# Kernel optimization log

Measured on AMD Instinct MI355X. Metric: run time of the kernel, lower is better.

The kernel has to match this reference:

```python
import jax, jax.numpy as jnp
import numpy as np

DIM = 192
HEADS = 4
HID = 576  # dim * ffn_expansion_factor
B, H, W = 8, 128, 128
EPS = 1e-5


def _conv(x, w, b, groups=1, pad=0):
    # x: NCHW, w: OIHW (I = in_channels // groups)
    out = jax.lax.conv_general_dilated(
        x, w, window_strides=(1, 1), padding=[(pad, pad), (pad, pad)],
        dimension_numbers=('NCHW', 'OIHW', 'NCHW'), feature_group_count=groups)
    return out + b[None, :, None, None]


def _layernorm(x, w, b):
    # WithBias LayerNorm over channel dim (equivalent to to_3d -> LN(last) -> to_4d)
    mu = jnp.mean(x, axis=1, keepdims=True)
    var = jnp.mean(jnp.square(x - mu), axis=1, keepdims=True)
    return (x - mu) / jnp.sqrt(var + EPS) * w[None, :, None, None] + b[None, :, None, None]


def _attention(x, qkv_w, qkv_b, qkv_dw_w, qkv_dw_b, temperature, prompt, proj_w, proj_b):
    b, c, h, w = x.shape
    qkv = _conv(_conv(x, qkv_w, qkv_b), qkv_dw_w, qkv_dw_b, groups=3 * DIM, pad=1)
    q, k, v = jnp.split(qkv, 3, axis=1)
    ch = c // HEADS
    hw = h * w
    q = q.reshape(b, HEADS, ch, hw) + prompt  # is_prompt=True: prompt added
    k = k.reshape(b, HEADS, ch, hw) + prompt
    v = v.reshape(b, HEADS, ch, hw) + prompt
    # L2 normalize along spatial (last) axis
    q = q / jnp.maximum(jnp.linalg.norm(q, axis=-1, keepdims=True), 1e-12)
    k = k / jnp.maximum(jnp.linalg.norm(k, axis=-1, keepdims=True), 1e-12)
    attn = jnp.einsum('bhcn,bhdn->bhcd', q, k) * temperature  # [b,heads,ch,ch]
    attn = jax.nn.softmax(attn, axis=-1)
    out = jnp.einsum('bhcd,bhdn->bhcn', attn, v)
    out = out.reshape(b, c, h, w)
    return _conv(out, proj_w, proj_b)


def _ffn(x, dw1_w, dw1_b, pm_w, pm_b, dw2_w, dw2_b, po_w, po_b):
    x1 = _conv(x, dw1_w, dw1_b, groups=DIM, pad=1)       # grouped 3x3: 192 -> 576
    x1 = _conv(x1, pm_w, pm_b)                            # 1x1: 576 -> 576
    x1 = jax.nn.gelu(x1, approximate=False)
    x2 = _conv(x1, dw2_w, dw2_b, groups=HID, pad=1)      # depthwise 3x3
    return _conv(x2, po_w, po_b)                          # 1x1: 576 -> 192


def setup_inputs() -> dict:
    key = jax.random.key(0)
    ks = jax.random.split(key, 24)
    rn = lambda i, shp, s=0.05: jax.random.normal(ks[i], shp, dtype=jnp.float32) * s
    return {
        'x': jax.random.normal(ks[0], (B, DIM, H, W), dtype=jnp.float32),
        'ln1_w': jnp.ones((DIM,), jnp.float32), 'ln1_b': jnp.zeros((DIM,), jnp.float32),
        'qkv_w': rn(1, (3 * DIM, DIM, 1, 1)), 'qkv_b': rn(2, (3 * DIM,)),
        'qkv_dw_w': rn(3, (3 * DIM, 1, 3, 3)), 'qkv_dw_b': rn(4, (3 * DIM,)),
        'temperature': jnp.ones((HEADS, 1, 1), jnp.float32),
        'prompt': jnp.ones((HEADS, DIM // HEADS, 1), jnp.float32),
        'proj_w': rn(5, (DIM, DIM, 1, 1)), 'proj_b': rn(6, (DIM,)),
        'ln2_w': jnp.ones((DIM,), jnp.float32), 'ln2_b': jnp.zeros((DIM,), jnp.float32),
        'ffn_dw1_w': rn(7, (HID, 1, 3, 3)), 'ffn_dw1_b': rn(8, (HID,)),
        'ffn_pm_w': rn(9, (HID, HID, 1, 1)), 'ffn_pm_b': rn(10, (HID,)),
        'ffn_dw2_w': rn(11, (HID, 1, 3, 3)), 'ffn_dw2_b': rn(12, (HID,)),
        'ffn_po_w': rn(13, (DIM, HID, 1, 1)), 'ffn_po_b': rn(14, (DIM,)),
    }


def reference(x, ln1_w, ln1_b, qkv_w, qkv_b, qkv_dw_w, qkv_dw_b, temperature, prompt,
              proj_w, proj_b, ln2_w, ln2_b, ffn_dw1_w, ffn_dw1_b, ffn_pm_w, ffn_pm_b,
              ffn_dw2_w, ffn_dw2_b, ffn_po_w, ffn_po_b):
    x = x + _attention(_layernorm(x, ln1_w, ln1_b), qkv_w, qkv_b, qkv_dw_w, qkv_dw_b,
                       temperature, prompt, proj_w, proj_b)
    x = x + _ffn(_layernorm(x, ln2_w, ln2_b), ffn_dw1_w, ffn_dw1_b, ffn_pm_w, ffn_pm_b,
                 ffn_dw2_w, ffn_dw2_b, ffn_po_w, ffn_po_b)
    return x
```

## Files before the change

### kernel.cpp

```cpp
#include <hip/hip_runtime.h>

#define HW     16384
#define NB     8
#define CDIM   192
#define CH3    576
#define NHEADS 4
#define CHH    48
#define NSL2   128
#define LDP    136
#define KT     64
#define LDK    72


typedef short  v8s  __attribute__((ext_vector_type(8)));
typedef float  v4f  __attribute__((ext_vector_type(4)));
typedef unsigned short u16x8 __attribute__((ext_vector_type(8)));

__device__ __forceinline__ float bf2f(unsigned short s) {
    return __uint_as_float(((unsigned)s) << 16);
}
__device__ __forceinline__ unsigned short f2bf(float f) {
    unsigned u = __float_as_uint(f);
    return (unsigned short)((u + 0x7fffu + ((u >> 16) & 1u)) >> 16);
}
__device__ __forceinline__ float gelu_f(float x) {
    return 0.5f * x * (1.0f + erff(x * 0.70710678118654752f));
}

__global__ __launch_bounds__(256) void wcvt(const float* __restrict__ s0,
                                            const float* __restrict__ s1,
                                            const float* __restrict__ s2,
                                            const float* __restrict__ s3,
                                            const float* __restrict__ dq,
                                            const float* __restrict__ d1,
                                            const float* __restrict__ d2,
                                            unsigned short* __restrict__ d,
                                            int n0, int n1, int n2, int n3) {
    int y = blockIdx.y;
    if (y < 4) {
        const float* srcs[4] = {s0, s1, s2, s3};
        int cnts[4] = {n0, n1, n2, n3};
        int offs[4] = {0, n0, n0 + n1, n0 + n1 + n2};
        const float* s = srcs[y];
        unsigned short* o = d + offs[y];
        int i = (blockIdx.x * 256 + threadIdx.x) * 8;
        if (i + 8 <= cnts[y]) {
            float4 a = *(const float4*)(s + i);
            float4 b = *(const float4*)(s + i + 4);
            u16x8 u;
            u[0] = f2bf(a.x); u[1] = f2bf(a.y); u[2] = f2bf(a.z); u[3] = f2bf(a.w);
            u[4] = f2bf(b.x); u[5] = f2bf(b.y); u[6] = f2bf(b.z); u[7] = f2bf(b.w);
            *(u16x8*)(o + i) = u;
        }
    } else {
        const float* s = (y == 4) ? dq : (y == 5) ? d1 : d2;
        unsigned short* o = d + (n0 + n1 + n2 + n3) + (y - 4) * 9 * CH3;
        int i = blockIdx.x * 256 + threadIdx.x;
        if (i < 9 * CH3) {
            int tap = i / CH3, c = i - tap * CH3;
            o[i] = f2bf(s[c * 9 + tap]);
        }
    }
}

__global__ __launch_bounds__(256) void zero_f(float* __restrict__ p, int n) {
    int i = blockIdx.x * 256 + threadIdx.x;
    if (i < n) p[i] = 0.f;
}

__global__ __launch_bounds__(256) void ln_norm(const float* __restrict__ x,
                                               const float* __restrict__ lnw,
                                               const float* __restrict__ lnb,
                                               unsigned short* __restrict__ xn) {
    int p = blockIdx.x * 256 + threadIdx.x;
    int z = blockIdx.y;
    const float* xp = x + (size_t)z * CDIM * HW;
    float s = 0.f, ss = 0.f;
    for (int c = 0; c < CDIM; ++c) {
        float v = xp[(size_t)c * HW + p];
        s += v; ss += v * v;
    }
    float m = s * (1.0f / CDIM);
    float var = ss * (1.0f / CDIM) - m * m;
    float r = 1.0f / sqrtf(var + 1e-5f);
    unsigned short* op = xn + (size_t)z * HW * CDIM;
    for (int cg = 0; cg < CDIM / 8; ++cg) {
        u16x8 u;
#pragma unroll
        for (int j = 0; j < 8; ++j) {
            int c = cg * 8 + j;
            u[j] = f2bf((xp[(size_t)c * HW + p] - m) * r * lnw[c] + lnb[c]);
        }
        *(u16x8*)(op + (size_t)cg * HW * 8 + (size_t)p * 8) = u;
    }
}

template <int EPI, int K>
__global__ __launch_bounds__(256) void gemm_c8(
    const unsigned short* __restrict__ Wb,
    const unsigned short* __restrict__ X,
    const float* __restrict__ bias,
    unsigned short* __restrict__ out) {
    __shared__ unsigned short Xs[128 * LDK];
    const int t = threadIdx.x;
    const int p0 = blockIdx.x * 128, M0 = blockIdx.y * 192, z = blockIdx.z;
    const int wid = t >> 6, lane = t & 63, lm = lane & 15, quad = lane >> 4;
    const int wp = (wid & 1) * 64, wc = (wid >> 1) * 96;

    const unsigned short* Xz = X + (size_t)z * HW * K;
    const int srow = t >> 1, shalf = (t & 1) * 32;
    const unsigned short* spz = Xz + (size_t)(p0 + srow) * 8;
    unsigned short* sd = &Xs[srow * LDK + shalf];

    v4f acc[4][6];
#pragma unroll
    for (int i = 0; i < 4; ++i)
#pragma unroll
        for (int j = 0; j < 6; ++j) acc[i][j] = (v4f)0.0f;

    const unsigned short* br[6];
#pragma unroll
    for (int j = 0; j < 6; ++j)
        br[j] = Wb + (size_t)(M0 + wc + j * 16 + lm) * K + quad * 8;

    for (int kt = 0; kt < K; kt += KT) {
        int cb = (kt + shalf) >> 3;
        u16x8 g0 = *(const u16x8*)(spz + (size_t)(cb + 0) * HW * 8);
        u16x8 g1 = *(const u16x8*)(spz + (size_t)(cb + 1) * HW * 8);
        u16x8 g2 = *(const u16x8*)(spz + (size_t)(cb + 2) * HW * 8);
        u16x8 g3 = *(const u16x8*)(spz + (size_t)(cb + 3) * HW * 8);
        if (kt) __syncthreads();
        *(u16x8*)sd = g0;
        *(u16x8*)(sd + 8) = g1;
        *(u16x8*)(sd + 16) = g2;
        *(u16x8*)(sd + 24) = g3;
        __syncthreads();
#pragma unroll
        for (int ks = 0; ks < 2; ++ks) {
            v8s a[4], b[6];
#pragma unroll
            for (int i = 0; i < 4; ++i)
                a[i] = *(const v8s*)&Xs[(wp + i * 16 + lm) * LDK + ks * 32 + quad * 8];
#pragma unroll
            for (int j = 0; j < 6; ++j)
                b[j] = *(const v8s*)(br[j] + kt + ks * 32);
#pragma unroll
            for (int i = 0; i < 4; ++i)
#pragma unroll
                for (int j = 0; j < 6; ++j)
                    acc[i][j] = __builtin_amdgcn_mfma_f32_16x16x32_bf16(a[i], b[j], acc[i][j], 0, 0, 0);
        }
    }

    unsigned short* Oz = out + (size_t)z * HW * (size_t)(EPI == 0 ? CH3 : CH3);
#pragma unroll
    for (int i = 0; i < 4; ++i)
#pragma unroll
        for (int j = 0; j < 6; ++j) {
            int ch = M0 + wc + j * 16 + lm;
            int cg = ch >> 3, co = ch & 7;
            float bch = bias[ch];
#pragma unroll
            for (int r = 0; r < 4; ++r) {
                int p = p0 + wp + i * 16 + quad * 4 + r;
                float v = acc[i][j][r] + bch;
                if (EPI == 1) v = gelu_f(v);
                Oz[(size_t)cg * HW * 8 + (size_t)p * 8 + co] = f2bf(v);
            }
        }
}

template <int K>
__global__ __launch_bounds__(256) void gemm_nchw(
    const unsigned short* __restrict__ Wb,
    const unsigned short* __restrict__ X,
    const float* __restrict__ bias,
    const float* __restrict__ res,
    float* __restrict__ outp) {
    __shared__ unsigned short Xs[128 * LDK];
    const int t = threadIdx.x;
    const int p0 = blockIdx.x * 128, z = blockIdx.z;
    const int wid = t >> 6, lane = t & 63, lm = lane & 15, quad = lane >> 4;
    const int wm = (wid >> 1) * 96, wph = (wid & 1) * 64;

    const unsigned short* Xz = X + (size_t)z * HW * K;
    const int srow = t >> 1, shalf = (t & 1) * 32;
    const unsigned short* spz = Xz + (size_t)(p0 + srow) * 8;
    unsigned short* sd = &Xs[srow * LDK + shalf];

    v4f acc[6][4];
#pragma unroll
    for (int i = 0; i < 6; ++i)
#pragma unroll
        for (int j = 0; j < 4; ++j) acc[i][j] = (v4f)0.0f;

    const unsigned short* ar[6];
#pragma unroll
    for (int i = 0; i < 6; ++i)
        ar[i] = Wb + (size_t)(wm + i * 16 + lm) * K + quad * 8;

    for (int kt = 0; kt < K; kt += KT) {
        int cb = (kt + shalf) >> 3;
        u16x8 g0 = *(const u16x8*)(spz + (size_t)(cb + 0) * HW * 8);
        u16x8 g1 = *(const u16x8*)(spz + (size_t)(cb + 1) * HW * 8);
        u16x8 g2 = *(const u16x8*)(spz + (size_t)(cb + 2) * HW * 8);
        u16x8 g3 = *(const u16x8*)(spz + (size_t)(cb + 3) * HW * 8);
        if (kt) __syncthreads();
        *(u16x8*)sd = g0;
        *(u16x8*)(sd + 8) = g1;
        *(u16x8*)(sd + 16) = g2;
        *(u16x8*)(sd + 24) = g3;
        __syncthreads();
#pragma unroll
        for (int ks = 0; ks < 2; ++ks) {
            v8s a[6], b[4];
#pragma unroll
            for (int i = 0; i < 6; ++i)
                a[i] = *(const v8s*)(ar[i] + kt + ks * 32);
#pragma unroll
            for (int j = 0; j < 4; ++j)
                b[j] = *(const v8s*)&Xs[(wph + j * 16 + lm) * LDK + ks * 32 + quad * 8];
#pragma unroll
            for (int i = 0; i < 6; ++i)
#pragma unroll
                for (int j = 0; j < 4; ++j)
                    acc[i][j] = __builtin_amdgcn_mfma_f32_16x16x32_bf16(a[i], b[j], acc[i][j], 0, 0, 0);
        }
    }

#pragma unroll
    for (int i = 0; i < 6; ++i)
#pragma unroll
        for (int j = 0; j < 4; ++j) {
            int gp = p0 + wph + j * 16 + lm;
#pragma unroll
            for (int r = 0; r < 4; ++r) {
                int gm = wm + i * 16 + quad * 4 + r;
                size_t oi = (size_t)z * CDIM * HW + (size_t)gm * HW + gp;
                outp[oi] = acc[i][j][r] + bias[gm] + res[oi];
            }
        }
}

__global__ __launch_bounds__(256) void dwp_c8(const unsigned short* __restrict__ in,
                                              const unsigned short* __restrict__ wT,
                                              const float* __restrict__ b1,
                                              const float* __restrict__ prompt,
                                              unsigned short* __restrict__ out,
                                              float* __restrict__ ssbuf) {
    int t = threadIdx.x;
    int px = blockIdx.x * 256 + t;
    int cg = blockIdx.y, c0 = cg * 8;
    int z = blockIdx.z;
    int h = px >> 7, w = px & 127;
    const unsigned short* ip = in + (size_t)z * HW * CH3 + (size_t)cg * HW * 8;
    int pc = c0 % CDIM;
    float acc[8];
#pragma unroll
    for (int j = 0; j < 8; ++j) acc[j] = b1[c0 + j] + prompt[pc + j];
#pragma unroll
    for (int ky = 0; ky < 3; ++ky) {
        int hy = h + ky - 1;
        if ((unsigned)hy >= 128u) continue;
#pragma unroll
        for (int kx = 0; kx < 3; ++kx) {
            int wx = w + kx - 1;
            if ((unsigned)wx >= 128u) continue;
            u16x8 xv = *(const u16x8*)(ip + (size_t)((hy << 7) + wx) * 8);
            u16x8 wv = *(const u16x8*)(wT + (ky * 3 + kx) * CH3 + c0);
#pragma unroll
            for (int j = 0; j < 8; ++j) acc[j] = fmaf(bf2f(wv[j]), bf2f(xv[j]), acc[j]);
        }
    }
    u16x8 o;
    float sl[8];
#pragma unroll
    for (int j = 0; j < 8; ++j) {
        unsigned short q = f2bf(acc[j]);
        o[j] = q;
        float vr = bf2f(q);
        sl[j] = vr * vr;
    }
    *(u16x8*)(out + (size_t)z * HW * CH3 + (size_t)cg * HW * 8 + (size_t)px * 8) = o;

    if (c0 < 384) {
        int wid = t >> 6, lane = t & 63;
#pragma unroll
        for (int j = 0; j < 8; ++j)
            for (int off = 32; off; off >>= 1) sl[j] += __shfl_down(sl[j], off);
        __shared__ float wr[4][8];
        if (lane == 0)
#pragma unroll
            for (int j = 0; j < 8; ++j) wr[wid][j] = sl[j];
        __syncthreads();
        if (t < 8) {
            float s = wr[0][t] + wr[1][t] + wr[2][t] + wr[3][t];
            atomicAdd(&ssbuf[z * 384 + c0 + t], s);
        }
    }
}

__global__ __launch_bounds__(256) void gram1(const unsigned short* __restrict__ qkvT,
                                             float* __restrict__ G0p) {
    const int sl = blockIdx.x, hh = blockIdx.y, z = blockIdx.z;
    const int t = threadIdx.x;
    const int wid = t >> 6, lane = t & 63, lm = lane & 15, quad = lane >> 4;

    __shared__ float Gs[4][2304];
    unsigned short* qs = (unsigned short*)&Gs[0][0];
    unsigned short* ks = qs + 48 * LDP;

    const unsigned short* bz = qkvT + (size_t)z * HW * CH3;
    int half = t & 1, pl = t >> 1;
    size_t pofs = (size_t)(sl * 128 + pl) * 8;
#pragma unroll
    for (int ci = 0; ci < 3; ++ci) {
        int cg = half * 3 + ci;
        u16x8 uq = *(const u16x8*)(bz + (size_t)(hh * 6 + cg) * HW * 8 + pofs);
        u16x8 uk = *(const u16x8*)(bz + (size_t)(24 + hh * 6 + cg) * HW * 8 + pofs);
#pragma unroll
        for (int j = 0; j < 8; ++j) {
            qs[(cg * 8 + j) * LDP + pl] = uq[j];
            ks[(cg * 8 + j) * LDP + pl] = uk[j];
        }
    }
    __syncthreads();

    v4f acc[3][3];
#pragma unroll
    for (int mi = 0; mi < 3; ++mi)
#pragma unroll
        for (int ni = 0; ni < 3; ++ni) acc[mi][ni] = (v4f)0.0f;

    int kp = wid * 32;
    v8s a[3], b[3];
#pragma unroll
    for (int i = 0; i < 3; ++i) {
        a[i] = *(const v8s*)&qs[(i * 16 + lm) * LDP + kp + quad * 8];
        b[i] = *(const v8s*)&ks[(i * 16 + lm) * LDP + kp + quad * 8];
    }
#pragma unroll
    for (int mi = 0; mi < 3; ++mi)
#pragma unroll
        for (int ni = 0; ni < 3; ++ni)
            acc[mi][ni] = __builtin_amdgcn_mfma_f32_16x16x32_bf16(a[mi], b[ni], acc[mi][ni], 0, 0, 0);

    __syncthreads();
#pragma unroll
    for (int mi = 0; mi < 3; ++mi)
#pragma unroll
        for (int ni = 0; ni < 3; ++ni)
#pragma unroll
            for (int r = 0; r < 4; ++r)
                Gs[wid][(mi * 16 + quad * 4 + r) * 48 + ni * 16 + lm] = acc[mi][ni][r];
    __syncthreads();
    float* gp = G0p + (((size_t)z * NHEADS + hh) * NSL2 + sl) * 2304;
    for (int i = t; i < 2304; i += 256)
        gp[i] = Gs[0][i] + Gs[1][i] + Gs[2][i] + Gs[3][i];
}

__global__ __launch_bounds__(256) void softmax1(const float* __restrict__ G0p,
                                                const float* __restrict__ ssbuf,
                                                const float* __restrict__ temp,
                                                unsigned short* __restrict__ Apad) {
    int hh = blockIdx.x, z = blockIdx.y, t = threadIdx.x;
    __shared__ float Gsum[2304];
    const float* gb = G0p + ((size_t)z * NHEADS + hh) * NSL2 * 2304;
    for (int i = t; i < 2304; i += 256) {
        float s = 0.f;
#pragma unroll 8
        for (int sl = 0; sl < NSL2; ++sl) s += gb[(size_t)sl * 2304 + i];
        Gsum[i] = s;
    }
    __syncthreads();
    if (t < 48) {
        float T = temp[hh];
        const float* sb = ssbuf + z * 384;
        float invq = 1.0f / fmaxf(sqrtf(sb[hh * CHH + t]), 1e-12f);
        float lg[48];
        float mx = -1e30f;
#pragma unroll
        for (int d = 0; d < 48; ++d) {
            float invk = 1.0f / fmaxf(sqrtf(sb[192 + hh * CHH + d]), 1e-12f);
            float l = T * Gsum[t * 48 + d] * invq * invk;
            lg[d] = l;
            mx = fmaxf(mx, l);
        }
        float sum = 0.f;
#pragma unroll
        for (int d = 0; d < 48; ++d) { float e = expf(lg[d] - mx); lg[d] = e; sum += e; }
        float inv = 1.0f / sum;
        unsigned short* ap = Apad + ((size_t)z * NHEADS + hh) * 48 * 64 + t * 64;
#pragma unroll
        for (int d = 0; d < 48; ++d) ap[d] = f2bf(lg[d] * inv);
#pragma unroll
        for (int d = 48; d < 64; ++d) ap[d] = 0;
    }
}

__global__ __launch_bounds__(256) void apply_pv(const unsigned short* __restrict__ qkvT,
                                                const unsigned short* __restrict__ Apad,
                                                unsigned short* __restrict__ attnout) {
    const int t = threadIdx.x;
    const int hh = blockIdx.y, z = blockIdx.z;
    const int wid = t >> 6, lane = t & 63, lm = lane & 15, quad = lane >> 4;
    const int p0 = blockIdx.x * 256 + wid * 64;

    const unsigned short* bz = qkvT + (size_t)z * HW * CH3;
    const unsigned short* Ab = Apad + ((size_t)z * NHEADS + hh) * 48 * 64;

    v4f acc[4][3];
#pragma unroll
    for (int i = 0; i < 4; ++i)
#pragma unroll
        for (int j = 0; j < 3; ++j) acc[i][j] = (v4f)0.0f;

#pragma unroll
    for (int ks = 0; ks < 2; ++ks) {
        int cgv = 48 + hh * 6 + ks * 4 + quad;
        if (cgv > 71) cgv = 71;
        const unsigned short* vp = bz + (size_t)cgv * HW * 8;
        v8s a[4], b[3];
#pragma unroll
        for (int i = 0; i < 4; ++i)
            a[i] = *(const v8s*)(vp + (size_t)(p0 + i * 16 + lm) * 8);
#pragma unroll
        for (int j = 0; j < 3; ++j)
            b[j] = *(const v8s*)(Ab + (j * 16 + lm) * 64 + ks * 32 + quad * 8);
#pragma unroll
        for (int i = 0; i < 4; ++i)
#pragma unroll
            for (int j = 0; j < 3; ++j)
                acc[i][j] = __builtin_amdgcn_mfma_f32_16x16x32_bf16(a[i], b[j], acc[i][j], 0, 0, 0);
    }

    unsigned short* Oz = attnout + (size_t)z * HW * CDIM;
#pragma unroll
    for (int i = 0; i < 4; ++i)
#pragma unroll
        for (int j = 0; j < 3; ++j) {
            int ch = hh * CHH + j * 16 + lm;
            int cg = ch >> 3, co = ch & 7;
#pragma unroll
            for (int r = 0; r < 4; ++r) {
                int p = p0 + i * 16 + quad * 4 + r;
                Oz[(size_t)cg * HW * 8 + (size_t)p * 8 + co] = f2bf(acc[i][j][r]);
            }
        }
}

__global__ __launch_bounds__(256) void dw1_c8(const unsigned short* __restrict__ xn,
                                              const unsigned short* __restrict__ wT,
                                              const float* __restrict__ b1,
                                              unsigned short* __restrict__ f1) {
    int t = threadIdx.x;
    int px = blockIdx.x * 256 + t;
    int gin = blockIdx.y;
    int c0 = gin * 24;
    int z = blockIdx.z;
    int h = px >> 7, w = px & 127;
    const unsigned short* ip = xn + (size_t)z * HW * CDIM + (size_t)gin * HW * 8;
    float acc[24];
#pragma unroll
    for (int j = 0; j < 24; ++j) acc[j] = b1[c0 + j];
#pragma unroll
    for (int ky = 0; ky < 3; ++ky) {
        int hy = h + ky - 1;
        if ((unsigned)hy >= 128u) continue;
#pragma unroll
        for (int kx = 0; kx < 3; ++kx) {
            int wx = w + kx - 1;
            if ((unsigned)wx >= 128u) continue;
            u16x8 xv = *(const u16x8*)(ip + (size_t)((hy << 7) + wx) * 8);
            float mv[8];
#pragma unroll
            for (int j = 0; j < 8; ++j) mv[j] = bf2f(xv[j]);
            const unsigned short* wp = wT + (ky * 3 + kx) * CH3 + c0;
            u16x8 w0 = *(const u16x8*)wp;
            u16x8 w1 = *(const u16x8*)(wp + 8);
            u16x8 w2 = *(const u16x8*)(wp + 16);
            float wv[24];
#pragma unroll
            for (int j = 0; j < 8; ++j) {
                wv[j] = bf2f(w0[j]); wv[8 + j] = bf2f(w1[j]); wv[16 + j] = bf2f(w2[j]);
            }
#pragma unroll
            for (int j = 0; j < 24; ++j) acc[j] = fmaf(wv[j], mv[j / 3], acc[j]);
        }
    }
    unsigned short* f1z = f1 + (size_t)z * HW * CH3;
#pragma unroll
    for (int q8 = 0; q8 < 3; ++q8) {
        u16x8 o;
#pragma unroll
        for (int j = 0; j < 8; ++j) o[j] = f2bf(acc[q8 * 8 + j]);
        *(u16x8*)(f1z + (size_t)(gin * 3 + q8) * HW * 8 + (size_t)px * 8) = o;
    }
}

__global__ __launch_bounds__(256) void dw2_c8(const unsigned short* __restrict__ in,
                                              const unsigned short* __restrict__ wT,
                                              const float* __restrict__ b1,
                                              unsigned short* __restrict__ out) {
    int t = threadIdx.x;
    int px = blockIdx.x * 256 + t;
    int cg = blockIdx.y, c0 = cg * 8;
    int z = blockIdx.z;
    int h = px >> 7, w = px & 127;
    const unsigned short* ip = in + (size_t)z * HW * CH3 + (size_t)cg * HW * 8;
    float acc[8];
#pragma unroll
    for (int j = 0; j < 8; ++j) acc[j] = b1[c0 + j];
#pragma unroll
    for (int ky = 0; ky < 3; ++ky) {
        int hy = h + ky - 1;
        if ((unsigned)hy >= 128u) continue;
#pragma unroll
        for (int kx = 0; kx < 3; ++kx) {
            int wx = w + kx - 1;
            if ((unsigned)wx >= 128u) continue;
            u16x8 xv = *(const u16x8*)(ip + (size_t)((hy << 7) + wx) * 8);
            u16x8 wv = *(const u16x8*)(wT + (ky * 3 + kx) * CH3 + c0);
#pragma unroll
            for (int j = 0; j < 8; ++j) acc[j] = fmaf(bf2f(wv[j]), bf2f(xv[j]), acc[j]);
        }
    }
    u16x8 o;
#pragma unroll
    for (int j = 0; j < 8; ++j) o[j] = f2bf(acc[j]);
    *(u16x8*)(out + (size_t)z * HW * CH3 + (size_t)cg * HW * 8 + (size_t)px * 8) = o;
}

extern "C" void kernel_launch(void* const* d_in, const int* in_sizes, int n_in,
                              void* d_out, int out_size, void* d_ws, size_t ws_size,
                              hipStream_t stream) {
    const float* x      = (const float*)d_in[0];
    const float* ln1w   = (const float*)d_in[1];
    const float* ln1b   = (const float*)d_in[2];
    const float* qkv_w  = (const float*)d_in[3];
    const float* qkv_b  = (const float*)d_in[4];
    const float* qdw_w  = (const float*)d_in[5];
    const float* qdw_b  = (const float*)d_in[6];
    const float* temp   = (const float*)d_in[7];
    const float* prompt = (const float*)d_in[8];
    const float* proj_w = (const float*)d_in[9];
    const float* proj_b = (const float*)d_in[10];
    const float* ln2w   = (const float*)d_in[11];
    const float* ln2b   = (const float*)d_in[12];
    const float* dw1_w  = (const float*)d_in[13];
    const float* dw1_b  = (const float*)d_in[14];
    const float* pm_w   = (const float*)d_in[15];
    const float* pm_b   = (const float*)d_in[16];
    const float* dw2_w  = (const float*)d_in[17];
    const float* dw2_b  = (const float*)d_in[18];
    const float* po_w   = (const float*)d_in[19];
    const float* po_b   = (const float*)d_in[20];
    float* out = (float*)d_out;
    (void)in_sizes; (void)n_in; (void)out_size;

    const int NWQ = CH3 * CDIM, NWP = CDIM * CDIM, NWM = CH3 * CH3, NWO = CDIM * CH3;
    const int NWALL = NWQ + NWP + NWM + NWO;

    auto al = [](size_t b) { return (b + 255) & ~(size_t)255; };
    auto need = [&](int PG) -> size_t {
        return 2 * al((size_t)PG * HW * CH3 * 2)
             + al((size_t)PG * HW * CDIM * 2)
             + al((size_t)PG * NHEADS * 48 * 64 * 2)
             + al((size_t)PG * 384 * 4)
             + al((size_t)(NWALL + 3 * 9 * CH3) * 2) + 4096;
    };
    int PG = 8;
    while (PG > 1 && need(PG) > ws_size) PG >>= 1;

    size_t off = 0;
    char* base = (char*)d_ws;
    auto alloc = [&](size_t bytes) -> char* {
        char* p = base + off;
        off = (off + bytes + 255) & ~(size_t)255;
        return p;
    };
    unsigned short* regionA = (unsigned short*)alloc((size_t)PG * HW * CH3 * 2);
    unsigned short* regionB = (unsigned short*)alloc((size_t)PG * HW * CH3 * 2);
    unsigned short* xng     = (unsigned short*)alloc((size_t)PG * HW * CDIM * 2);
    unsigned short* Apad    = (unsigned short*)alloc((size_t)PG * NHEADS * 48 * 64 * 2);
    float*          ssbuf   = (float*)alloc((size_t)PG * 384 * 4);
    unsigned short* wbf     = (unsigned short*)alloc((size_t)(NWALL + 3 * 9 * CH3) * 2);

    unsigned short* wq   = wbf;
    unsigned short* wpj  = wbf + NWQ;
    unsigned short* wpm  = wbf + NWQ + NWP;
    unsigned short* wpo  = wbf + NWQ + NWP + NWM;
    unsigned short* wdwT = wbf + NWALL;
    unsigned short* wd1T = wdwT + 9 * CH3;
    unsigned short* wd2T = wd1T + 9 * CH3;

    unsigned short* preQKV  = regionA;
    unsigned short* attnout = regionA;
    unsigned short* f1      = regionA;
    unsigned short* f3      = regionA;
    unsigned short* qkvT    = regionB;
    unsigned short* f2      = regionB;
    float* G0p = (float*)xng;

    dim3 blk(256);

    wcvt<<<dim3(162, 7), blk, 0, stream>>>(qkv_w, proj_w, pm_w, po_w,
                                           qdw_w, dw1_w, dw2_w,
                                           wbf, NWQ, NWP, NWM, NWO);

    for (int b0 = 0; b0 < NB; b0 += PG) {
        const float* xb = x + (size_t)b0 * CDIM * HW;
        float* x2b      = out + (size_t)b0 * CDIM * HW;

        zero_f<<<dim3((PG * 384 + 255) / 256), blk, 0, stream>>>(ssbuf, PG * 384);
        ln_norm<<<dim3(64, PG), blk, 0, stream>>>(xb, ln1w, ln1b, xng);
        gemm_c8<0, CDIM><<<dim3(128, 3, PG), blk, 0, stream>>>(
            wq, xng, qkv_b, preQKV);
        dwp_c8<<<dim3(64, 72, PG), blk, 0, stream>>>(
            preQKV, wdwT, qdw_b, prompt, qkvT, ssbuf);
        gram1<<<dim3(NSL2, NHEADS, PG), blk, 0, stream>>>(qkvT, G0p);
        softmax1<<<dim3(NHEADS, PG), blk, 0, stream>>>(G0p, ssbuf, temp, Apad);
        apply_pv<<<dim3(64, NHEADS, PG), blk, 0, stream>>>(qkvT, Apad, attnout);
        gemm_nchw<CDIM><<<dim3(128, 1, PG), blk, 0, stream>>>(
            wpj, attnout, proj_b, xb, x2b);

        ln_norm<<<dim3(64, PG), blk, 0, stream>>>(x2b, ln2w, ln2b, xng);
        dw1_c8<<<dim3(64, 24, PG), blk, 0, stream>>>(xng, wd1T, dw1_b, f1);
        gemm_c8<1, CH3><<<dim3(128, 3, PG), blk, 0, stream>>>(
            wpm, f1, pm_b, f2);
        dw2_c8<<<dim3(64, 72, PG), blk, 0, stream>>>(f2, wd2T, dw2_b, f3);
        gemm_nchw<CH3><<<dim3(128, 1, PG), blk, 0, stream>>>(
            wpo, f3, po_b, x2b, x2b);
    }
}
```

Before: 1.226 ms.

## Prepack GEMM weights into MFMA fragment order and load activations directly from global

After: 1.121 ms. 8.6% less time.

```diff
diff --git a/kernel.cpp b/kernel.cpp
--- a/kernel.cpp
+++ b/kernel.cpp
@@ -8,8 +8,6 @@
 #define CHH    48
 #define NSL2   128
 #define LDP    136
-#define KT     64
-#define LDK    72
 
 
 typedef short  v8s  __attribute__((ext_vector_type(8)));
@@ -39,18 +37,27 @@
     int y = blockIdx.y;
     if (y < 4) {
         const float* srcs[4] = {s0, s1, s2, s3};
-        int cnts[4] = {n0, n1, n2, n3};
+        const int Ms[4] = {CH3, CDIM, CH3, CDIM};
+        const int Ks[4] = {CDIM, CDIM, CH3, CH3};
         int offs[4] = {0, n0, n0 + n1, n0 + n1 + n2};
         const float* s = srcs[y];
         unsigned short* o = d + offs[y];
-        int i = (blockIdx.x * 256 + threadIdx.x) * 8;
-        if (i + 8 <= cnts[y]) {
-            float4 a = *(const float4*)(s + i);
-            float4 b = *(const float4*)(s + i + 4);
+        int M = Ms[y], K = Ks[y];
+        int i = blockIdx.x * 256 + threadIdx.x;
+        int total = M * K / 8;
+        if (i < total) {
+            int tiles_k = K / 32;
+            int tm = i / (tiles_k * 64);
+            int rem = i - tm * (tiles_k * 64);
+            int tk = rem >> 6, lane = rem & 63;
+            int quad = lane >> 4, lm = lane & 15;
+            const float* sp = s + (size_t)(tm * 16 + lm) * K + tk * 32 + quad * 8;
+            float4 a = *(const float4*)sp;
+            float4 b = *(const float4*)(sp + 4);
             u16x8 u;
             u[0] = f2bf(a.x); u[1] = f2bf(a.y); u[2] = f2bf(a.z); u[3] = f2bf(a.w);
             u[4] = f2bf(b.x); u[5] = f2bf(b.y); u[6] = f2bf(b.z); u[7] = f2bf(b.w);
-            *(u16x8*)(o + i) = u;
+            *(u16x8*)(o + (size_t)i * 8) = u;
         }
     } else {
         const float* s = (y == 4) ? dq : (y == 5) ? d1 : d2;
@@ -97,20 +104,19 @@
 
 template <int EPI, int K>
 __global__ __launch_bounds__(256) void gemm_c8(
-    const unsigned short* __restrict__ Wb,
+    const unsigned short* __restrict__ Wp,
     const unsigned short* __restrict__ X,
     const float* __restrict__ bias,
     unsigned short* __restrict__ out) {
-    __shared__ unsigned short Xs[128 * LDK];
     const int t = threadIdx.x;
     const int p0 = blockIdx.x * 128, M0 = blockIdx.y * 192, z = blockIdx.z;
     const int wid = t >> 6, lane = t & 63, lm = lane & 15, quad = lane >> 4;
     const int wp = (wid & 1) * 64, wc = (wid >> 1) * 96;
+    constexpr int TK = K / 32;
 
     const unsigned short* Xz = X + (size_t)z * HW * K;
-    const int srow = t >> 1, shalf = (t & 1) * 32;
-    const unsigned short* spz = Xz + (size_t)(p0 + srow) * 8;
-    unsigned short* sd = &Xs[srow * LDK + shalf];
+    const unsigned short* xa = Xz + (size_t)(p0 + wp + lm) * 8 + (size_t)quad * HW * 8;
+    const unsigned short* bw = Wp + ((size_t)((M0 + wc) >> 4) * TK) * 512 + lane * 8;
 
     v4f acc[4][6];
 #pragma unroll
@@ -118,41 +124,24 @@
 #pragma unroll
         for (int j = 0; j < 6; ++j) acc[i][j] = (v4f)0.0f;
 
-    const unsigned short* br[6];
-#pragma unroll
-    for (int j = 0; j < 6; ++j)
-        br[j] = Wb + (size_t)(M0 + wc + j * 16 + lm) * K + quad * 8;
-
-    for (int kt = 0; kt < K; kt += KT) {
-        int cb = (kt + shalf) >> 3;
-        u16x8 g0 = *(const u16x8*)(spz + (size_t)(cb + 0) * HW * 8);
-        u16x8 g1 = *(const u16x8*)(spz + (size_t)(cb + 1) * HW * 8);
-        u16x8 g2 = *(const u16x8*)(spz + (size_t)(cb + 2) * HW * 8);
-        u16x8 g3 = *(const u16x8*)(spz + (size_t)(cb + 3) * HW * 8);
-        if (kt) __syncthreads();
-        *(u16x8*)sd = g0;
-        *(u16x8*)(sd + 8) = g1;
-        *(u16x8*)(sd + 16) = g2;
-        *(u16x8*)(sd + 24) = g3;
-        __syncthreads();
-#pragma unroll
-        for (int ks = 0; ks < 2; ++ks) {
-            v8s a[4], b[6];
-#pragma unroll
-            for (int i = 0; i < 4; ++i)
-                a[i] = *(const v8s*)&Xs[(wp + i * 16 + lm) * LDK + ks * 32 + quad * 8];
+#pragma unroll 2
+    for (int kt = 0; kt < K; kt += 32) {
+        const unsigned short* xk = xa + (size_t)(kt >> 3) * HW * 8;
+        v8s a[4], b[6];
+#pragma unroll
+        for (int i = 0; i < 4; ++i)
+            a[i] = *(const v8s*)(xk + i * 128);
+#pragma unroll
+        for (int j = 0; j < 6; ++j)
+            b[j] = *(const v8s*)(bw + ((size_t)j * TK + (kt >> 5)) * 512);
+#pragma unroll
+        for (int i = 0; i < 4; ++i)
 #pragma unroll
             for (int j = 0; j < 6; ++j)
-                b[j] = *(const v8s*)(br[j] + kt + ks * 32);
-#pragma unroll
-            for (int i = 0; i < 4; ++i)
-#pragma unroll
-                for (int j = 0; j < 6; ++j)
-                    acc[i][j] = __builtin_amdgcn_mfma_f32_16x16x32_bf16(a[i], b[j], acc[i][j], 0, 0, 0);
-        }
-    }
-
-    unsigned short* Oz = out + (size_t)z * HW * (size_t)(EPI == 0 ? CH3 : CH3);
+                acc[i][j] = __builtin_amdgcn_mfma_f32_16x16x32_bf16(a[i], b[j], acc[i][j], 0, 0, 0);
+    }
+
+    unsigned short* Oz = out + (size_t)z * HW * CH3;
 #pragma unroll
     for (int i = 0; i < 4; ++i)
 #pragma unroll
@@ -172,21 +161,20 @@
 
 template <int K>
 __global__ __launch_bounds__(256) void gemm_nchw(
-    const unsigned short* __restrict__ Wb,
+    const unsigned short* __restrict__ Wp,
     const unsigned short* __restrict__ X,
     const float* __restrict__ bias,
     const float* __restrict__ res,
     float* __restrict__ outp) {
-    __shared__ unsigned short Xs[128 * LDK];
     const int t = threadIdx.x;
     const int p0 = blockIdx.x * 128, z = blockIdx.z;
     const int wid = t >> 6, lane = t & 63, lm = lane & 15, quad = lane >> 4;
     const int wm = (wid >> 1) * 96, wph = (wid & 1) * 64;
+    constexpr int TK = K / 32;
 
     const unsigned short* Xz = X + (size_t)z * HW * K;
-    const int srow = t >> 1, shalf = (t & 1) * 32;
-    const unsigned short* spz = Xz + (size_t)(p0 + srow) * 8;
-    unsigned short* sd = &Xs[srow * LDK + shalf];
+    const unsigned short* xb = Xz + (size_t)(p0 + wph + lm) * 8 + (size_t)quad * HW * 8;
+    const unsigned short* aw = Wp + ((size_t)(wm >> 4) * TK) * 512 + lane * 8;
 
     v4f acc[6][4];
 #pragma unroll
@@ -194,38 +182,21 @@
 #pragma unroll
         for (int j = 0; j < 4; ++j) acc[i][j] = (v4f)0.0f;
 
-    const unsigned short* ar[6];
-#pragma unroll
-    for (int i = 0; i < 6; ++i)
-        ar[i] = Wb + (size_t)(wm + i * 16 + lm) * K + quad * 8;
-
-    for (int kt = 0; kt < K; kt += KT) {
-        int cb = (kt + shalf) >> 3;
-        u16x8 g0 = *(const u16x8*)(spz + (size_t)(cb + 0) * HW * 8);
-        u16x8 g1 = *(const u16x8*)(spz + (size_t)(cb + 1) * HW * 8);
-        u16x8 g2 = *(const u16x8*)(spz + (size_t)(cb + 2) * HW * 8);
-        u16x8 g3 = *(const u16x8*)(spz + (size_t)(cb + 3) * HW * 8);
-        if (kt) __syncthreads();
-        *(u16x8*)sd = g0;
-        *(u16x8*)(sd + 8) = g1;
-        *(u16x8*)(sd + 16) = g2;
-        *(u16x8*)(sd + 24) = g3;
-        __syncthreads();
-#pragma unroll
-        for (int ks = 0; ks < 2; ++ks) {
-            v8s a[6], b[4];
-#pragma unroll
-            for (int i = 0; i < 6; ++i)
-                a[i] = *(const v8s*)(ar[i] + kt + ks * 32);
+#pragma unroll 2
+    for (int kt = 0; kt < K; kt += 32) {
+        const unsigned short* xk = xb + (size_t)(kt >> 3) * HW * 8;
+        v8s a[6], b[4];
+#pragma unroll
+        for (int i = 0; i < 6; ++i)
+            a[i] = *(const v8s*)(aw + ((size_t)i * TK + (kt >> 5)) * 512);
+#pragma unroll
+        for (int j = 0; j < 4; ++j)
+            b[j] = *(const v8s*)(xk + j * 128);
+#pragma unroll
+        for (int i = 0; i < 6; ++i)
 #pragma unroll
             for (int j = 0; j < 4; ++j)
-                b[j] = *(const v8s*)&Xs[(wph + j * 16 + lm) * LDK + ks * 32 + quad * 8];
-#pragma unroll
-            for (int i = 0; i < 6; ++i)
-#pragma unroll
-                for (int j = 0; j < 4; ++j)
-                    acc[i][j] = __builtin_amdgcn_mfma_f32_16x16x32_bf16(a[i], b[j], acc[i][j], 0, 0, 0);
-        }
+                acc[i][j] = __builtin_amdgcn_mfma_f32_16x16x32_bf16(a[i], b[j], acc[i][j], 0, 0, 0);
     }
 
 #pragma unroll
```
